# Kernel tuning notes

Hardware: AMD Instinct MI355X
Metric: run time of the kernel (lower is better)

## Reference

```python
import jax, jax.numpy as jnp
import numpy as np

B, C, T = 32, 32, 1024
K = 64          # kernel_size
DIL = 1         # dilation
MLP_DIM = 256
HID = 256       # mlp_hidden_dim; TanhBlock dims: 256 -> 256 -> 128 -> 1
NF = min(MLP_DIM, K // 2 + 1)          # 33 rfft bins kept
FFT_DIM = C * NF * 2                   # 2112
N_WIN = T - DIL * (K - 1)              # 961 windows


def setup_inputs() -> dict:
    key = jax.random.key(0)
    ks = jax.random.split(key, 8)
    s = 0.02
    return {
        "x": jax.random.normal(ks[0], (B, C, T), dtype=jnp.float32),
        "Wp": jax.random.normal(ks[1], (MLP_DIM, FFT_DIM), dtype=jnp.float32) * s,
        "bp": jnp.zeros((MLP_DIM,), dtype=jnp.float32),
        "W1": jax.random.normal(ks[2], (HID, MLP_DIM), dtype=jnp.float32) * s,
        "b1": jnp.zeros((HID,), dtype=jnp.float32),
        "W2": jax.random.normal(ks[3], (HID // 2, HID), dtype=jnp.float32) * s,
        "b2": jnp.zeros((HID // 2,), dtype=jnp.float32),
        "Wout": jax.random.normal(ks[4], (1, HID // 2), dtype=jnp.float32) * s,
        "bout": jnp.zeros((1,), dtype=jnp.float32),
        "agg": jnp.zeros((N_WIN,), dtype=jnp.float32),
    }


def reference(x, Wp, bp, W1, b1, W2, b2, Wout, bout, agg):
    # Gather all dilated windows at once: window t uses indices (t-start)+k*DIL.
    base = jnp.arange(N_WIN)[:, None] + jnp.arange(K)[None, :] * DIL  # [W, K]
    win = x[:, :, base]                          # [B, C, W, K]
    fft = jnp.fft.rfft(win, axis=-1)[..., :NF]   # [B, C, W, NF] complex
    mag = jnp.log1p(jnp.abs(fft))
    ph = jnp.angle(fft) / np.pi
    feat = jnp.stack([mag, ph], axis=-1)         # [B, C, W, NF, 2]
    # torch reshape order is (C, NF, 2) -> move window axis before channel
    feat = feat.transpose(0, 2, 1, 3, 4).reshape(B, N_WIN, FFT_DIM)  # [B, W, FFT_DIM]
    proj = jnp.tanh(feat @ Wp.T + bp) * np.pi    # [B, W, MLP_DIM]
    h = jnp.tanh(proj @ W1.T + b1)               # [B, W, HID]
    h = jnp.tanh(h @ W2.T + b2)                  # [B, W, HID//2]
    out = (h @ Wout.T + bout)[..., 0]            # [B, W]
    wts = jax.nn.softmax(agg)                    # [W]
    return (out * wts[None, :]).sum(axis=1)      # [B]
```

## Files before the change

### kernel.cpp

```cpp
#include <hip/hip_runtime.h>
#include <math.h>

#define B_   32
#define C_   32
#define T_   1024
#define NF_  33
#define F2_  66
#define FD_  2112
#define FDH_ 1056
#define NW_  961
#define MLP_ 256
#define HID_ 256
#define HH_  128
#define TN_  32
#define NT_  31

#define PI_F     3.14159265358979323846f
#define LN2_F    0.69314718055994530942f
#define L2E2_F   2.88539008177792681472f

typedef unsigned short u16;
typedef unsigned int   u32;
typedef __attribute__((ext_vector_type(8))) short bf16x8;
typedef __attribute__((ext_vector_type(4))) float f32x4;

__device__ __forceinline__ u16 f2bf(float f) {
    u32 u = __float_as_uint(f);
    u = u + 0x7FFFu + ((u >> 16) & 1u);
    return (u16)(u >> 16);
}
__device__ __forceinline__ u32 pk_bf16(float lo, float hi) {
    u32 r;
    asm("v_cvt_pk_bf16_f32 %0, %1, %2" : "=v"(r) : "v"(lo), "v"(hi));
    return r;
}
__device__ __forceinline__ void gload16(const void* g, void* l) {
    __builtin_amdgcn_global_load_lds(
        (const __attribute__((address_space(1))) void*)g,
        (__attribute__((address_space(3))) void*)l, 16, 0, 0);
}
__device__ __forceinline__ float ftanh(float x) {
    float z = __builtin_amdgcn_exp2f(x * L2E2_F);
    return 1.f - 2.f * __builtin_amdgcn_rcpf(z + 1.f);
}
__device__ __forceinline__ float flog1p(float x) {
    return __builtin_amdgcn_logf(1.f + x) * LN2_F;
}
__device__ __forceinline__ float fatan2pi(float y, float x) {
    const float ay = fabsf(y), ax = fabsf(x);
    const float mn = fminf(ay, ax), mx = fmaxf(ay, ax);
    float t = mn * __builtin_amdgcn_rcpf(mx);
    t = (mx == 0.f) ? 0.f : t;
    const float s = t * t;
    float p = -0.027097f;
    p = fmaf(p, s,  0.057337f);
    p = fmaf(p, s, -0.105130f);
    p = fmaf(p, s,  0.318268f);
    p *= t;
    p = (ay > ax) ? 0.5f - p : p;
    p = (x < 0.f) ? 1.0f - p : p;
    return copysignf(p, y);
}

__global__ __launch_bounds__(256) void prep_kernel(
        const float* __restrict__ Wp, const float* __restrict__ W1,
        const float* __restrict__ W2, const float* __restrict__ agg,
        u16* __restrict__ WpP, u16* __restrict__ W1H, u16* __restrict__ W2H,
        float* __restrict__ wts) {
    const int blk = blockIdx.x;
    const int tid = threadIdx.x;
    if (blk < 128) {
        const int total = MLP_ * FD_;
        for (int i = blk * 256 + tid; i < total; i += 128 * 256) {
            const int n = i / FD_;
            const int k = i - n * FD_;
            const int c = k / F2_;
            const int q = k - c * F2_;
            const int kp = (q < 64) ? (c * 64 + q) : (2048 + 2 * c + (q - 64));
            WpP[(size_t)n * FD_ + kp] = f2bf(Wp[i]);
        }
    } else if (blk < 160) {
        const int total = HID_ * MLP_;
        for (int i = (blk - 128) * 256 + tid; i < total; i += 32 * 256)
            W1H[i] = f2bf(W1[i]);
    } else if (blk < 176) {
        const int total = HH_ * HID_;
        for (int i = (blk - 160) * 256 + tid; i < total; i += 16 * 256)
            W2H[i] = f2bf(W2[i]);
    } else {
        __shared__ float red[256];
        float mx = -INFINITY;
        for (int i = tid; i < NW_; i += 256) mx = fmaxf(mx, agg[i]);
        red[tid] = mx; __syncthreads();
        for (int s = 128; s > 0; s >>= 1) {
            if (tid < s) red[tid] = fmaxf(red[tid], red[tid + s]);
            __syncthreads();
        }
        mx = red[0]; __syncthreads();
        float sm = 0.f;
        for (int i = tid; i < NW_; i += 256) sm += expf(agg[i] - mx);
        red[tid] = sm; __syncthreads();
        for (int s = 128; s > 0; s >>= 1) {
            if (tid < s) red[tid] += red[tid + s];
            __syncthreads();
        }
        const float inv = 1.f / red[0];
        for (int i = tid; i < NW_; i += 256) wts[i] = expf(agg[i] - mx) * inv;
    }
}

__global__ __launch_bounds__(256) void feat_kernel(const float* __restrict__ x,
                                                   u32* __restrict__ featP) {
    const int n0 = blockIdx.x * TN_;
    const int cg = blockIdx.y;
    const int bb = blockIdx.z;
    const int tid = threadIdx.x;
    const int tf = tid & 31;
    const int c8 = tid >> 5;
    const int c  = cg * 8 + c8;

    __shared__ float2 stab[64];
    __shared__ float xs[8][96];
    __shared__ float basisT[64][66];

    if (tid < 64) {
        float s, cc;
        sincosf(-PI_F * (float)tid / 32.0f, &s, &cc);
        stab[tid] = make_float2(cc, s);
    }
    __syncthreads();
    for (int e = tid; e < 2048; e += 256) {
        const int f = e >> 6, k = e & 63;
        const float2 w = stab[(f * k) & 63];
        basisT[k][2 * f]     = w.x;
        basisT[k][2 * f + 1] = w.y;
    }
    if (tid < 192) {
        const int cs = tid / 24, q = tid % 24;
        const int t0 = n0 + q * 4;
        const float* xb = x + ((size_t)bb * C_ + cg * 8 + cs) * T_;
        float4 v;
        if (t0 + 3 < T_) {
            v = *(const float4*)(xb + t0);
        } else {
            v.x = (t0 + 0 < T_) ? xb[t0 + 0] : 0.f;
            v.y = (t0 + 1 < T_) ? xb[t0 + 1] : 0.f;
            v.z = (t0 + 2 < T_) ? xb[t0 + 2] : 0.f;
            v.w = 0.f;
        }
        *(float4*)&xs[cs][q * 4] = v;
    }
    __syncthreads();

    const size_t rowb = (size_t)bb * NW_;

    {
        float re = 0.f, im = 0.f;
#pragma unroll
        for (int k = 0; k < 64; ++k) {
            const float xv = xs[c8][k];
            const float2 w = *(const float2*)&basisT[k][2 * tf];
            re = fmaf(xv, w.x, re);
            im = fmaf(xv, w.y, im);
        }
        const float2 st = stab[tf];
        const float cx = st.x, sx = -st.y;

        u32* fp = featP + (rowb + n0) * FDH_ + (c << 5) + tf;
        const int nw = (NW_ - n0 < TN_) ? (NW_ - n0) : TN_;
        for (int j = 0; j < nw; ++j) {
            const float r   = __builtin_amdgcn_sqrtf(fmaf(re, re, im * im));
            const float mag = flog1p(r);
            const float ph  = fatan2pi(im, re);
            *fp = pk_bf16(mag, ph);
            fp += FDH_;
            const float tre = re - xs[c8][j] + xs[c8][j + 64];
            re = tre * cx - im * sx;
            im = tre * sx + im * cx;
        }
    }

    {
        const int j   = tid & 31;
        const int c8n = tid >> 5;
        const int gn  = n0 + j;
        if (gn < NW_) {
            float s = 0.f;
#pragma unroll
            for (int k = 0; k < 32; ++k)
                s += xs[c8n][j + 2 * k] - xs[c8n][j + 2 * k + 1];
            const float a = flog1p(fabsf(s));
            const float p = (__float_as_uint(s) >> 31) ? 1.0f : 0.0f;
            featP[(rowb + gn) * FDH_ + 1024 + cg * 8 + c8n] = pk_bf16(a, p);
        }
    }
}

__global__ __launch_bounds__(512, 1) void gemm64_kernel(
        const u16* __restrict__ A, const u16* __restrict__ BH,
        const float* __restrict__ bias, float scale,
        u16* __restrict__ outH, int Mvalid, int Kd) {
    constexpr int STEPB = 16384 + 32768;
    __shared__ char lds[3 * STEPB];

    const int bm = blockIdx.x;
    const int tid = threadIdx.x;
    const int lane = tid & 63, w = tid >> 6;
    const int wr = w >> 2, wc = w & 3;
    const int m0 = bm * 128;

    f32x4 acc[4][4];
#pragma unroll
    for (int i = 0; i < 4; ++i)
#pragma unroll
        for (int j = 0; j < 4; ++j) acc[i][j] = (f32x4){0.f, 0.f, 0.f, 0.f};

    const size_t rs = (size_t)Kd * 2;
    const char* gA = (const char*)A + (size_t)m0 * rs;
    const char* gB = (const char*)BH;

    auto st1 = [&](const char* g, char* l, int idx) {
        const int row = idx >> 3;
        const int kc  = (idx & 7) ^ ((row >> 1) & 7);
        gload16(g + (size_t)row * rs + (size_t)(kc << 4), l + idx * 16);
    };
    auto stage = [&](int buf, int t) {
        const size_t k0b = (size_t)t << 7;
        char* lb = lds + buf * STEPB;
        st1(gA + k0b, lb, tid);
        st1(gA + k0b, lb, tid + 512);
        st1(gB + k0b, lb + 16384, tid);
        st1(gB + k0b, lb + 16384, tid + 512);
        st1(gB + k0b, lb + 16384, tid + 1024);
        st1(gB + k0b, lb + 16384, tid + 1536);
    };

    const int q   = lane >> 4;
    const int ra_ = wr * 64 + (lane & 15);
    const int rb_ = wc * 64 + (lane & 15);
    const int s3a = (ra_ >> 1) & 7;
    const int s3b = (rb_ >> 1) & 7;
    const int ab0 = ra_ * 128 + (((0 * 4 + q) ^ s3a) << 4);
    const int ab1 = ra_ * 128 + (((1 * 4 + q) ^ s3a) << 4);
    const int bb0 = rb_ * 128 + (((0 * 4 + q) ^ s3b) << 4);
    const int bb1 = rb_ * 128 + (((1 * 4 + q) ^ s3b) << 4);

    const int nt = Kd >> 6;

    stage(0, 0);
    stage(1, 1);

    int cur = 0;
    for (int t = 0; t < nt; ++t) {
        if (t + 1 < nt)
            asm volatile("s_waitcnt vmcnt(6)" ::: "memory");
        else
            asm volatile("s_waitcnt vmcnt(0)" ::: "memory");
        __builtin_amdgcn_sched_barrier(0);
        __builtin_amdgcn_s_barrier();
        asm volatile("" ::: "memory");

        int pf = cur + 2; if (pf >= 3) pf -= 3;
        if (t + 2 < nt) stage(pf, t + 2);

        const char* lb = lds + cur * STEPB;
        bf16x8 a0[4], a1[4], b0[4], b1[4];
#pragma unroll
        for (int f = 0; f < 4; ++f) {
            a0[f] = *(const bf16x8*)(lb + ab0 + f * 2048);
            a1[f] = *(const bf16x8*)(lb + ab1 + f * 2048);
            b0[f] = *(const bf16x8*)(lb + 16384 + bb0 + f * 2048);
            b1[f] = *(const bf16x8*)(lb + 16384 + bb1 + f * 2048);
        }
        __builtin_amdgcn_s_setprio(1);
#pragma unroll
        for (int fm = 0; fm < 4; ++fm)
#pragma unroll
            for (int fn = 0; fn < 4; ++fn)
                acc[fm][fn] = __builtin_amdgcn_mfma_f32_16x16x32_bf16(a0[fm], b0[fn], acc[fm][fn], 0, 0, 0);
#pragma unroll
        for (int fm = 0; fm < 4; ++fm)
#pragma unroll
            for (int fn = 0; fn < 4; ++fn)
                acc[fm][fn] = __builtin_amdgcn_mfma_f32_16x16x32_bf16(a1[fm], b1[fn], acc[fm][fn], 0, 0, 0);
        __builtin_amdgcn_s_setprio(0);
        ++cur; if (cur >= 3) cur -= 3;
    }

    float bv[4];
#pragma unroll
    for (int fn = 0; fn < 4; ++fn) bv[fn] = bias[wc * 64 + fn * 16 + (lane & 15)];
#pragma unroll
    for (int fm = 0; fm < 4; ++fm) {
        const int rbase = m0 + wr * 64 + fm * 16 + (lane >> 4) * 4;
#pragma unroll
        for (int fn = 0; fn < 4; ++fn) {
            const int col = wc * 64 + fn * 16 + (lane & 15);
#pragma unroll
            for (int r = 0; r < 4; ++r) {
                const int row = rbase + r;
                if (row < Mvalid) {
                    const float v = ftanh(acc[fm][fn][r] + bv[fn]) * scale;
                    outH[(size_t)row * 256 + col] = f2bf(v);
                }
            }
        }
    }
}

__global__ __launch_bounds__(512, 1) void mlp_tail_kernel(
        const u16* __restrict__ A, const u16* __restrict__ W1Hp,
        const float* __restrict__ b1, const u16* __restrict__ W2Hp,
        const float* __restrict__ b2, const float* __restrict__ Wout,
        const float* __restrict__ bout, const float* __restrict__ wts,
        float* __restrict__ partial, int Mvalid) {
    constexpr int STEPB = 8192 + 16384;
    constexpr int OFFX  = 3 * STEPB;
    __shared__ char lds[OFFX + 65536];

    const int bm = blockIdx.x;
    const int tid = threadIdx.x;
    const int lane = tid & 63, w = tid >> 6;
    const int m0 = bm * 128;
    const size_t rs = 512;

    {
        const int wr = w >> 2, wc = w & 3;
        f32x4 acc[4][4];
#pragma unroll
        for (int i = 0; i < 4; ++i)
#pragma unroll
            for (int j = 0; j < 4; ++j) acc[i][j] = (f32x4){0.f, 0.f, 0.f, 0.f};

        const char* gA = (const char*)A + (size_t)m0 * rs;
        const char* gB = (const char*)W1Hp;

        auto st1 = [&](const char* g, char* l, int idx) {
            const int row = idx >> 2;
            const int kc  = (idx & 3) ^ ((row >> 1) & 3);
            gload16(g + (size_t)row * rs + (size_t)(kc << 4), l + idx * 16);
        };
        auto stage = [&](int buf, int t) {
            const size_t k0b = (size_t)t << 6;
            char* lb = lds + buf * STEPB;
            st1(gA + k0b, lb, tid);
            st1(gB + k0b, lb + 8192, tid);
            st1(gB + k0b, lb + 8192, tid + 512);
        };

        const int ra_ = wr * 64 + (lane & 15);
        const int rb_ = wc * 64 + (lane & 15);
        const int q   = lane >> 4;
        const int abase = ra_ * 64 + ((q ^ ((ra_ >> 1) & 3)) << 4);
        const int bbase = rb_ * 64 + ((q ^ ((rb_ >> 1) & 3)) << 4);

        stage(0, 0);
        stage(1, 1);

        int cur = 0;
        for (int t = 0; t < 8; ++t) {
            if (t + 1 < 8)
                asm volatile("s_waitcnt vmcnt(3)" ::: "memory");
            else
                asm volatile("s_waitcnt vmcnt(0)" ::: "memory");
            __builtin_amdgcn_sched_barrier(0);
            __builtin_amdgcn_s_barrier();
            asm volatile("" ::: "memory");

            int pf = cur + 2; if (pf >= 3) pf -= 3;
            if (t + 2 < 8) stage(pf, t + 2);

            const char* lb = lds + cur * STEPB;
            bf16x8 a4[4], b4[4];
#pragma unroll
            for (int f = 0; f < 4; ++f) {
                a4[f] = *(const bf16x8*)(lb + abase + f * 1024);
                b4[f] = *(const bf16x8*)(lb + 8192 + bbase + f * 1024);
            }
            __builtin_amdgcn_s_setprio(1);
#pragma unroll
            for (int fm = 0; fm < 4; ++fm)
#pragma unroll
                for (int fn = 0; fn < 4; ++fn)
                    acc[fm][fn] = __builtin_amdgcn_mfma_f32_16x16x32_bf16(a4[fm], b4[fn], acc[fm][fn], 0, 0, 0);
            __builtin_amdgcn_s_setprio(0);
            ++cur; if (cur >= 3) cur -= 3;
        }

        float bv[4];
#pragma unroll
        for (int fn = 0; fn < 4; ++fn) bv[fn] = b1[wc * 64 + fn * 16 + (lane & 15)];
#pragma unroll
        for (int fm = 0; fm < 4; ++fm) {
#pragma unroll
            for (int fn = 0; fn < 4; ++fn) {
                const int col = wc * 64 + fn * 16 + (lane & 15);
                const int cpart = ((col >> 5) << 6) + ((col & 7) * 2);
                const int kc = (col >> 3) & 3;
#pragma unroll
                for (int r = 0; r < 4; ++r) {
                    const int row = wr * 64 + fm * 16 + (lane >> 4) * 4 + r;
                    const float v = ftanh(acc[fm][fn][r] + bv[fn]);
                    const int byt = row * 512 + cpart + ((kc ^ ((row >> 1) & 3)) << 4);
                    *(u16*)(lds + OFFX + byt) = f2bf(v);
                }
            }
        }
    }
    __syncthreads();

    f32x4 acc2[4][4];
#pragma unroll
    for (int i = 0; i < 4; ++i)
#pragma unroll
        for (int j = 0; j < 4; ++j) acc2[i][j] = (f32x4){0.f, 0.f, 0.f, 0.f};

    const int wr2 = (w >> 1) & 1, wc2 = w & 1;
    {
        const char* gB2 = (const char*)W2Hp;
        auto st2 = [&](int buf, int t) {
            const size_t k0b = (size_t)t << 6;
            const int row = tid >> 2;
            const int kc  = (tid & 3) ^ ((row >> 1) & 3);
            gload16(gB2 + (size_t)row * rs + k0b + (size_t)(kc << 4),
                    lds + buf * STEPB + tid * 16);
        };
        st2(0, 0);
        st2(1, 1);

        const int q = lane >> 4;
        const int rb = wc2 * 64 + (lane & 15);
        const int bbase = rb * 64 + ((q ^ ((rb >> 1) & 3)) << 4);
        const int ra = wr2 * 64 + (lane & 15);
        const int abase = ra * 512 + ((q ^ ((ra >> 1) & 3)) << 4);

        int cur = 0;
        for (int t = 0; t < 8; ++t) {
            if (t + 1 < 8)
                asm volatile("s_waitcnt vmcnt(1)" ::: "memory");
            else
                asm volatile("s_waitcnt vmcnt(0)" ::: "memory");
            __builtin_amdgcn_sched_barrier(0);
            __builtin_amdgcn_s_barrier();
            asm volatile("" ::: "memory");

            int pf = cur + 2; if (pf >= 3) pf -= 3;
            if (t + 2 < 8) st2(pf, t + 2);

            if (w < 4) {
                const char* lb = lds + cur * STEPB;
                bf16x8 a4[4], b4[4];
#pragma unroll
                for (int f = 0; f < 4; ++f) {
                    a4[f] = *(const bf16x8*)(lds + OFFX + abase + f * 8192 + t * 64);
                    b4[f] = *(const bf16x8*)(lb + bbase + f * 1024);
                }
                __builtin_amdgcn_s_setprio(1);
#pragma unroll
                for (int fm = 0; fm < 4; ++fm)
#pragma unroll
                    for (int fn = 0; fn < 4; ++fn)
                        acc2[fm][fn] = __builtin_amdgcn_mfma_f32_16x16x32_bf16(a4[fm], b4[fn], acc2[fm][fn], 0, 0, 0);
                __builtin_amdgcn_s_setprio(0);
            }
            ++cur; if (cur >= 3) cur -= 3;
        }
    }

    __syncthreads();
    float* rsum = (float*)lds;
    float* red  = (float*)(lds + 1024);

    if (w < 4) {
        float bv[4], wv[4];
#pragma unroll
        for (int fn = 0; fn < 4; ++fn) {
            const int col = wc2 * 64 + fn * 16 + (lane & 15);
            bv[fn] = b2[col];
            wv[fn] = Wout[col];
        }
#pragma unroll
        for (int fm = 0; fm < 4; ++fm) {
#pragma unroll
            for (int r = 0; r < 4; ++r) {
                float c = 0.f;
#pragma unroll
                for (int fn = 0; fn < 4; ++fn)
                    c += ftanh(acc2[fm][fn][r] + bv[fn]) * wv[fn];
                c += __shfl_xor(c, 1);
                c += __shfl_xor(c, 2);
                c += __shfl_xor(c, 4);
                c += __shfl_xor(c, 8);
                if ((lane & 15) == 0)
                    rsum[(wr2 * 64 + fm * 16 + (lane >> 4) * 4 + r) * 2 + wc2] = c;
            }
        }
    }
    __syncthreads();

    const float bO = bout[0];
    float val = 0.f;
    int rowb = -1;
    if (tid < 128) {
        const int gr = m0 + tid;
        if (gr < Mvalid) {
            const float dot = rsum[tid * 2] + rsum[tid * 2 + 1] + bO;
            rowb = gr / NW_;
            val = dot * wts[gr - rowb * NW_];
        }
    }
    __syncthreads();

    const int bFirst = m0 / NW_;
    if (tid < 256) red[tid] = (tid < 128 && rowb == bFirst) ? val : 0.f;
    __syncthreads();
    for (int s = 128; s > 0; s >>= 1) {
        if (tid < s) red[tid] += red[tid + s];
        __syncthreads();
    }
    if (tid == 0) partial[bm * 2] = red[0];
    __syncthreads();
    if (tid < 256) red[tid] = (tid < 128 && rowb == bFirst + 1) ? val : 0.f;
    __syncthreads();
    for (int s = 128; s > 0; s >>= 1) {
        if (tid < s) red[tid] += red[tid + s];
        __syncthreads();
    }
    if (tid == 0) partial[bm * 2 + 1] = red[0];
}

__global__ __launch_bounds__(64) void finred_kernel(const float* __restrict__ partial,
                                                    float* __restrict__ out,
                                                    int nbat, int nblocks) {
    const int b = threadIdx.x;
    if (b >= nbat) return;
    int lo = (b * NW_) / 128;
    int hi = ((b + 1) * NW_ - 1) / 128;
    if (hi > nblocks - 1) hi = nblocks - 1;
    float s = 0.f;
    for (int bm = lo; bm <= hi; ++bm) {
        const int slot = ((bm * 128) / NW_ == b) ? 0 : 1;
        s += partial[bm * 2 + slot];
    }
    out[b] = s;
}

extern "C" void kernel_launch(void* const* d_in, const int* in_sizes, int n_in,
                              void* d_out, int out_size, void* d_ws, size_t ws_size,
                              hipStream_t stream) {
    const float* x    = (const float*)d_in[0];
    const float* Wp   = (const float*)d_in[1];
    const float* bp   = (const float*)d_in[2];
    const float* W1   = (const float*)d_in[3];
    const float* b1   = (const float*)d_in[4];
    const float* W2   = (const float*)d_in[5];
    const float* b2   = (const float*)d_in[6];
    const float* Wout = (const float*)d_in[7];
    const float* bout = (const float*)d_in[8];
    const float* agg  = (const float*)d_in[9];
    float* out = (float*)d_out;

    char* wsb = (char*)d_ws;
    size_t off = 0;
    auto ra = [](size_t b) { return (b + 255) & ~(size_t)255; };
    auto alloc = [&](size_t bytes) -> char* {
        char* p = wsb + off;
        off += ra(bytes);
        return p;
    };

    u16* WpP = (u16*)alloc((size_t)MLP_ * FD_ * 2);
    u16* W1H = (u16*)alloc((size_t)HID_ * MLP_ * 2);
    u16* W2H = (u16*)alloc((size_t)HH_ * HID_ * 2);
    float* wts = (float*)alloc((size_t)NW_ * 4);

    const size_t fixed = off;
    int NB = 32;
    for (;;) {
        const size_t M = (size_t)NB * NW_;
        const size_t Mp = ((M + 127) / 128) * 128;
        const size_t need = ra(Mp * FD_ * 2) +
                            ra(Mp * 256 * 2) +
                            ra((Mp / 128) * 2 * 4);
        if (fixed + need <= ws_size || NB == 1) break;
        NB >>= 1;
    }
    const size_t Mmax  = (size_t)NB * NW_;
    const size_t MpMax = ((Mmax + 127) / 128) * 128;
    u16* featH = (u16*)alloc(MpMax * FD_ * 2);
    u16* projH = (u16*)alloc(MpMax * 256 * 2);
    float* partial = (float*)alloc((MpMax / 128) * 2 * 4);

    prep_kernel<<<dim3(177), dim3(256), 0, stream>>>(
        Wp, W1, W2, agg, WpP, W1H, W2H, wts);

    for (int b0 = 0; b0 < B_; b0 += NB) {
        const int nb = (B_ - b0 < NB) ? (B_ - b0) : NB;
        const int M = nb * NW_;
        const int Mp = ((M + 127) / 128) * 128;

        feat_kernel<<<dim3(NT_, 4, nb), dim3(256), 0, stream>>>(
            x + (size_t)b0 * C_ * T_, (u32*)featH);

        gemm64_kernel<<<dim3(Mp / 128), dim3(512), 0, stream>>>(
            featH, WpP, bp, PI_F, projH, M, FD_);

        mlp_tail_kernel<<<dim3(Mp / 128), dim3(512), 0, stream>>>(
            projH, W1H, b1, W2H, b2, Wout, bout, wts, partial, M);

        finred_kernel<<<dim3(1), dim3(64), 0, stream>>>(
            partial, out + b0, nb, Mp / 128);
    }
}
```

Before: 119.3 us.

## Fuse weight-prep into feature kernel and double window tile per block

Merges the weight conversion/softmax prep kernel and the FFT feature kernel into one launch, with the first 177 blocks doing prep and the rest computing features. Each feature block now handles 64 windows instead of 32, so the per-block basis table setup is amortized over more windows and the grid shrinks. This drops one kernel launch and lets prep overlap feature work. The cost is a longer serial sliding-DFT chain per thread. If the batch loop runs more than once, the prep work is redundantly repeated each iteration.

Measured after the change: 111.1 us, median of 2. -6.9%, faster.

```diff
diff --git a/kernel.cpp b/kernel.cpp
--- a/kernel.cpp
+++ b/kernel.cpp
@@ -12,8 +12,8 @@
 #define MLP_ 256
 #define HID_ 256
 #define HH_  128
-#define TN_  32
-#define NT_  31
+#define TN_  64
+#define NT_  16
 
 #define PI_F     3.14159265358979323846f
 #define LN2_F    0.69314718055994530942f
@@ -62,65 +62,68 @@
     return copysignf(p, y);
 }
 
-__global__ __launch_bounds__(256) void prep_kernel(
+__global__ __launch_bounds__(256) void prepfeat_kernel(
+        const float* __restrict__ x,
         const float* __restrict__ Wp, const float* __restrict__ W1,
         const float* __restrict__ W2, const float* __restrict__ agg,
         u16* __restrict__ WpP, u16* __restrict__ W1H, u16* __restrict__ W2H,
-        float* __restrict__ wts) {
+        float* __restrict__ wts, u32* __restrict__ featP) {
     const int blk = blockIdx.x;
     const int tid = threadIdx.x;
-    if (blk < 128) {
-        const int total = MLP_ * FD_;
-        for (int i = blk * 256 + tid; i < total; i += 128 * 256) {
-            const int n = i / FD_;
-            const int k = i - n * FD_;
-            const int c = k / F2_;
-            const int q = k - c * F2_;
-            const int kp = (q < 64) ? (c * 64 + q) : (2048 + 2 * c + (q - 64));
-            WpP[(size_t)n * FD_ + kp] = f2bf(Wp[i]);
-        }
-    } else if (blk < 160) {
-        const int total = HID_ * MLP_;
-        for (int i = (blk - 128) * 256 + tid; i < total; i += 32 * 256)
-            W1H[i] = f2bf(W1[i]);
-    } else if (blk < 176) {
-        const int total = HH_ * HID_;
-        for (int i = (blk - 160) * 256 + tid; i < total; i += 16 * 256)
-            W2H[i] = f2bf(W2[i]);
-    } else {
-        __shared__ float red[256];
-        float mx = -INFINITY;
-        for (int i = tid; i < NW_; i += 256) mx = fmaxf(mx, agg[i]);
-        red[tid] = mx; __syncthreads();
-        for (int s = 128; s > 0; s >>= 1) {
-            if (tid < s) red[tid] = fmaxf(red[tid], red[tid + s]);
-            __syncthreads();
-        }
-        mx = red[0]; __syncthreads();
-        float sm = 0.f;
-        for (int i = tid; i < NW_; i += 256) sm += expf(agg[i] - mx);
-        red[tid] = sm; __syncthreads();
-        for (int s = 128; s > 0; s >>= 1) {
-            if (tid < s) red[tid] += red[tid + s];
-            __syncthreads();
-        }
-        const float inv = 1.f / red[0];
-        for (int i = tid; i < NW_; i += 256) wts[i] = expf(agg[i] - mx) * inv;
-    }
-}
-
-__global__ __launch_bounds__(256) void feat_kernel(const float* __restrict__ x,
-                                                   u32* __restrict__ featP) {
-    const int n0 = blockIdx.x * TN_;
-    const int cg = blockIdx.y;
-    const int bb = blockIdx.z;
-    const int tid = threadIdx.x;
-    const int tf = tid & 31;
-    const int c8 = tid >> 5;
-    const int c  = cg * 8 + c8;
+
+    if (blk < 177) {
+        if (blk < 128) {
+            const int total = MLP_ * FD_;
+            for (int i = blk * 256 + tid; i < total; i += 128 * 256) {
+                const int n = i / FD_;
+                const int k = i - n * FD_;
+                const int c = k / F2_;
+                const int q = k - c * F2_;
+                const int kp = (q < 64) ? (c * 64 + q) : (2048 + 2 * c + (q - 64));
+                WpP[(size_t)n * FD_ + kp] = f2bf(Wp[i]);
+            }
+        } else if (blk < 160) {
+            const int total = HID_ * MLP_;
+            for (int i = (blk - 128) * 256 + tid; i < total; i += 32 * 256)
+                W1H[i] = f2bf(W1[i]);
+        } else if (blk < 176) {
+            const int total = HH_ * HID_;
+            for (int i = (blk - 160) * 256 + tid; i < total; i += 16 * 256)
+                W2H[i] = f2bf(W2[i]);
+        } else {
+            __shared__ float red[256];
+            float mx = -INFINITY;
+            for (int i = tid; i < NW_; i += 256) mx = fmaxf(mx, agg[i]);
+            red[tid] = mx; __syncthreads();
+            for (int s = 128; s > 0; s >>= 1) {
+                if (tid < s) red[tid] = fmaxf(red[tid], red[tid + s]);
+                __syncthreads();
+            }
+            mx = red[0]; __syncthreads();
+            float sm = 0.f;
+            for (int i = tid; i < NW_; i += 256) sm += expf(agg[i] - mx);
+            red[tid] = sm; __syncthreads();
+            for (int s = 128; s > 0; s >>= 1) {
+                if (tid < s) red[tid] += red[tid + s];
+                __syncthreads();
+            }
+            const float inv = 1.f / red[0];
+            for (int i = tid; i < NW_; i += 256) wts[i] = expf(agg[i] - mx) * inv;
+        }
+        return;
+    }
+
+    const int fb  = blk - 177;
+    const int bb  = fb >> 6;
+    const int r2  = fb & 63;
+    const int cg  = r2 >> 4;
+    const int n0  = (r2 & 15) * TN_;
+    const int tf  = tid & 31;
+    const int c8  = tid >> 5;
+    const int c   = cg * 8 + c8;
 
     __shared__ float2 stab[64];
-    __shared__ float xs[8][96];
+    __shared__ float xs[8][128];
     __shared__ float basisT[64][66];
 
     if (tid < 64) {
@@ -135,18 +138,17 @@
         basisT[k][2 * f]     = w.x;
         basisT[k][2 * f + 1] = w.y;
     }
-    if (tid < 192) {
-        const int cs = tid / 24, q = tid % 24;
+    {
+        const int cs = tid >> 5, q = tid & 31;
         const int t0 = n0 + q * 4;
         const float* xb = x + ((size_t)bb * C_ + cg * 8 + cs) * T_;
-        float4 v;
+        float4 v = {0.f, 0.f, 0.f, 0.f};
         if (t0 + 3 < T_) {
             v = *(const float4*)(xb + t0);
         } else {
-            v.x = (t0 + 0 < T_) ? xb[t0 + 0] : 0.f;
-            v.y = (t0 + 1 < T_) ? xb[t0 + 1] : 0.f;
-            v.z = (t0 + 2 < T_) ? xb[t0 + 2] : 0.f;
-            v.w = 0.f;
+            if (t0 + 0 < T_) v.x = xb[t0 + 0];
+            if (t0 + 1 < T_) v.y = xb[t0 + 1];
+            if (t0 + 2 < T_) v.z = xb[t0 + 2];
         }
         *(float4*)&xs[cs][q * 4] = v;
     }
@@ -181,17 +183,20 @@
     }
 
     {
-        const int j   = tid & 31;
         const int c8n = tid >> 5;
-        const int gn  = n0 + j;
-        if (gn < NW_) {
-            float s = 0.f;
-#pragma unroll
-            for (int k = 0; k < 32; ++k)
-                s += xs[c8n][j + 2 * k] - xs[c8n][j + 2 * k + 1];
-            const float a = flog1p(fabsf(s));
-            const float p = (__float_as_uint(s) >> 31) ? 1.0f : 0.0f;
-            featP[(rowb + gn) * FDH_ + 1024 + cg * 8 + c8n] = pk_bf16(a, p);
+#pragma unroll
+        for (int half = 0; half < 2; ++half) {
+            const int j  = (tid & 31) + half * 32;
+            const int gn = n0 + j;
+            if (gn < NW_) {
+                float s = 0.f;
+#pragma unroll
+                for (int k = 0; k < 32; ++k)
+                    s += xs[c8n][j + 2 * k] - xs[c8n][j + 2 * k + 1];
+                const float a = flog1p(fabsf(s));
+                const float p = (__float_as_uint(s) >> 31) ? 1.0f : 0.0f;
+                featP[(rowb + gn) * FDH_ + 1024 + cg * 8 + c8n] = pk_bf16(a, p);
+            }
         }
     }
 }
@@ -591,16 +596,14 @@
     u16* projH = (u16*)alloc(MpMax * 256 * 2);
     float* partial = (float*)alloc((MpMax / 128) * 2 * 4);
 
-    prep_kernel<<<dim3(177), dim3(256), 0, stream>>>(
-        Wp, W1, W2, agg, WpP, W1H, W2H, wts);
-
     for (int b0 = 0; b0 < B_; b0 += NB) {
         const int nb = (B_ - b0 < NB) ? (B_ - b0) : NB;
         const int M = nb * NW_;
         const int Mp = ((M + 127) / 128) * 128;
 
-        feat_kernel<<<dim3(NT_, 4, nb), dim3(256), 0, stream>>>(
-            x + (size_t)b0 * C_ * T_, (u32*)featH);
+        prepfeat_kernel<<<dim3(177 + 64 * nb), dim3(256), 0, stream>>>(
+            x + (size_t)b0 * C_ * T_, Wp, W1, W2, agg,
+            WpP, W1H, W2H, wts, (u32*)featH);
 
         gemm64_kernel<<<dim3(Mp / 128), dim3(512), 0, stream>>>(
             featH, WpP, bp, PI_F, projH, M, FD_);
```
